# Kernel optimization log

Hardware: AMD Instinct MI355X
Metric: run time of the kernel (lower is better)

The kernel has to match this reference:

```python
import jax, jax.numpy as jnp
import numpy as np

N = 50000; FIN = 64; H = 128; E = 800000; T = 8
P = 250000; D = 500000; G = 20000; V = 2000; O = 2


def _mp(h, Ws, Wn, b, edge_src, edge_dst, n):
    # mean-aggregation message passing: relu(h Ws + mean_neigh(h) Wn + b)
    deg = jax.ops.segment_sum(jnp.ones(edge_dst.shape[0], h.dtype), edge_dst, n)
    agg = jax.ops.segment_sum(h[edge_src], edge_dst, n) / jnp.maximum(deg, 1.0)[:, None]
    return jax.nn.relu(h @ Ws + agg @ Wn + b)


def _forward(x, W_enc_self, W_enc_nei, b_enc, W2_self, W2_nei, b2, Wd1, bd1, Wd2, bd2,
             counts, edge_src, edge_dst, place_idx, src_idx, t_idx, dst_nodes, dst_seg,
             group_id, variant_of_group):
    n = x.shape[0]
    p = place_idx.shape[0]
    g = variant_of_group.shape[0]
    v = counts.shape[0]
    # first encoder, then T sequential second_encoder applications (feature generations)
    h0 = _mp(x, W_enc_self, W_enc_nei, b_enc, edge_src, edge_dst, n)

    def step(h, _):
        h2 = _mp(h, W2_self, W2_nei, b2, edge_src, edge_dst, n)
        return h2, h2

    _, hs = jax.lax.scan(step, h0, None, length=T)
    feats = jnp.concatenate([h0[None], hs], axis=0)  # [T+1, N, H]

    # gather (place, src) features at the generation index of each prediction
    place_f = feats[t_idx, place_idx]                 # [P, H]
    src_f = feats[t_idx, src_idx]                     # [P, H]
    # dst feature = sum over the destination set of each prediction
    dst_f = jax.ops.segment_sum(feats[t_idx[dst_seg], dst_nodes], dst_seg, p)  # [P, H]

    cat = jnp.concatenate([place_f, src_f, dst_f], axis=-1)  # [P, 3H]
    logits = jax.nn.relu(cat @ Wd1 + bd1) @ Wd2 + bd2        # [P, O]
    logprob = jax.nn.log_softmax(logits, axis=-1)            # [P, O]

    # prev_prob: inclusive running sum of per-step logprob sums within each variant
    group_sums = jax.ops.segment_sum(logprob, group_id, g)   # [G, O]
    cum = jnp.cumsum(group_sums, axis=0)
    var_tot = jax.ops.segment_sum(group_sums, variant_of_group, v)
    var_excl = jnp.cumsum(var_tot, axis=0) - var_tot
    within = cum - var_excl[variant_of_group]                # [G, O]
    prev = within[group_id]                                  # [P, O]

    logc = jnp.log(counts / jnp.sum(counts))                 # log(count/total) per variant
    add = logprob + prev + logc[variant_of_group[group_id]][:, None]
    return jnp.zeros((n, logits.shape[-1]), x.dtype).at[place_idx].add(add)


def setup_inputs() -> dict:
    ks = jax.random.split(jax.random.key(0), 24)
    s = jnp.float32(0.05)
    f32 = jnp.float32
    i32 = jnp.int32
    return {
        "x": jax.random.normal(ks[0], (N, FIN), f32),
        "W_enc_self": jax.random.normal(ks[1], (FIN, H), f32) * s,
        "W_enc_nei": jax.random.normal(ks[2], (FIN, H), f32) * s,
        "b_enc": jax.random.normal(ks[3], (H,), f32) * s,
        "W2_self": jax.random.normal(ks[4], (H, H), f32) * s,
        "W2_nei": jax.random.normal(ks[5], (H, H), f32) * s,
        "b2": jax.random.normal(ks[6], (H,), f32) * s,
        "Wd1": jax.random.normal(ks[7], (3 * H, 3 * H), f32) * s,
        "bd1": jax.random.normal(ks[8], (3 * H,), f32) * s,
        "Wd2": jax.random.normal(ks[9], (3 * H, O), f32) * s,
        "bd2": jax.random.normal(ks[10], (O,), f32) * s,
        "counts": jax.random.uniform(ks[11], (V,), f32) + 0.5,
        "edge_src": jax.random.randint(ks[12], (E,), 0, N, i32),
        "edge_dst": jax.random.randint(ks[13], (E,), 0, N, i32),
        "place_idx": jax.random.randint(ks[14], (P,), 0, N, i32),
        "src_idx": jax.random.randint(ks[15], (P,), 0, N, i32),
        "t_idx": jax.random.randint(ks[16], (P,), 0, T + 1, i32),
        "dst_nodes": jax.random.randint(ks[17], (D,), 0, N, i32),
        "dst_seg": jnp.sort(jax.random.randint(ks[18], (D,), 0, P, i32)),
        "group_id": jnp.sort(jax.random.randint(ks[19], (P,), 0, G, i32)),
        "variant_of_group": jnp.sort(jax.random.randint(ks[20], (G,), 0, V, i32)),
    }


def reference(x, W_enc_self, W_enc_nei, b_enc, W2_self, W2_nei, b2, Wd1, bd1, Wd2, bd2,
              counts, edge_src, edge_dst, place_idx, src_idx, t_idx, dst_nodes, dst_seg,
              group_id, variant_of_group):
    return _forward(x, W_enc_self, W_enc_nei, b_enc, W2_self, W2_nei, b2, Wd1, bd1, Wd2, bd2,
                    counts, edge_src, edge_dst, place_idx, src_idx, t_idx, dst_nodes, dst_seg,
                    group_id, variant_of_group)
```

## Files before the change

### kernel.cpp

```cpp
#include <hip/hip_runtime.h>
#include <math.h>

#define NN 50000
#define FINN 64
#define HD 128
#define EE 800000
#define TT 8
#define PP 250000
#define DD 500000
#define GG 20000
#define VV 2000
#define OO 2

#define DEC_GRID 256
#define DEC_TILES ((PP + 63) / 64)

typedef short short8 __attribute__((ext_vector_type(8)));
typedef float f32x4 __attribute__((ext_vector_type(4)));

__device__ __forceinline__ unsigned short f2bf(float f) {
    unsigned int u = __float_as_uint(f);
    u += 0x7fffu + ((u >> 16) & 1u);
    return (unsigned short)(u >> 16);
}
__device__ __forceinline__ float bf2f(unsigned short u) {
    return __uint_as_float(((unsigned int)u) << 16);
}

struct us8 { unsigned short v[8]; };

__device__ __forceinline__ void gload_lds16(const void* g, void* l) {
    __builtin_amdgcn_global_load_lds((__attribute__((address_space(1))) void*)g,
                                     (__attribute__((address_space(3))) void*)l, 16, 0, 0);
}

__global__ void count_k(const int* __restrict__ idx, int* __restrict__ counts, int n) {
    int i = blockIdx.x * blockDim.x + threadIdx.x;
    if (i < n) atomicAdd(&counts[idx[i]], 1);
}

__global__ void blk_sum_k(const int* __restrict__ counts, int n, int* __restrict__ bsum) {
    __shared__ int buf[256];
    int t = threadIdx.x, i = blockIdx.x * 256 + t;
    buf[t] = (i < n) ? counts[i] : 0;
    __syncthreads();
    for (int off = 128; off > 0; off >>= 1) {
        if (t < off) buf[t] += buf[t + off];
        __syncthreads();
    }
    if (t == 0) bsum[blockIdx.x] = buf[0];
}

__global__ void scan_small_k(const int* __restrict__ bsum, int nb, int* __restrict__ boff) {
    __shared__ int buf[256];
    int t = threadIdx.x;
    int v = (t < nb) ? bsum[t] : 0;
    buf[t] = v;
    __syncthreads();
    for (int off = 1; off < 256; off <<= 1) {
        int u = (t >= off) ? buf[t - off] : 0;
        __syncthreads();
        buf[t] += u;
        __syncthreads();
    }
    if (t < nb) boff[t] = buf[t] - v;
}

__global__ void rowptr_fill_k(const int* __restrict__ counts, const int* __restrict__ boff,
                              int n, int* __restrict__ rowptr, int total) {
    __shared__ int buf[256];
    int t = threadIdx.x, i = blockIdx.x * 256 + t;
    int v = (i < n) ? counts[i] : 0;
    buf[t] = v;
    __syncthreads();
    for (int off = 1; off < 256; off <<= 1) {
        int u = (t >= off) ? buf[t - off] : 0;
        __syncthreads();
        buf[t] += u;
        __syncthreads();
    }
    if (i < n) rowptr[i] = boff[blockIdx.x] + buf[t] - v;
    if (i == 0) rowptr[n] = total;
}

__global__ void lb_rowptr_k(const int* __restrict__ arr, int n, int* __restrict__ rowptr, int m) {
    int i = blockIdx.x * blockDim.x + threadIdx.x;
    if (i > m) return;
    int lo = 0, hi = n;
    while (lo < hi) {
        int mid = (lo + hi) >> 1;
        if (arr[mid] < i) lo = mid + 1; else hi = mid;
    }
    rowptr[i] = lo;
}

__global__ void fill_csr_k(const int* __restrict__ esrc, const int* __restrict__ edst,
                           const int* __restrict__ rowptr, int* __restrict__ cursor,
                           int* __restrict__ outi, int n) {
    int e = blockIdx.x * blockDim.x + threadIdx.x;
    if (e < n) {
        int d = edst[e];
        int pos = atomicAdd(&cursor[d], 1);
        outi[rowptr[d] + pos] = esrc[e];
    }
}

__global__ void hist9_k(const int* __restrict__ t_idx, int* __restrict__ hist) {
    __shared__ int l[9];
    if (threadIdx.x < 9) l[threadIdx.x] = 0;
    __syncthreads();
    int p = blockIdx.x * 256 + threadIdx.x;
    if (p < PP) atomicAdd(&l[t_idx[p]], 1);
    __syncthreads();
    if (threadIdx.x < 9) atomicAdd(&hist[threadIdx.x], l[threadIdx.x]);
}

__global__ void scan9_k(const int* __restrict__ hist, int* __restrict__ boff9) {
    if (threadIdx.x == 0) {
        int a = 0;
        for (int i = 0; i < 9; ++i) { boff9[i] = a; a += hist[i]; }
    }
}

__global__ void bucket_perm_k(const int* __restrict__ t_idx, const int* __restrict__ boff9,
                              int* __restrict__ cursor9, int* __restrict__ pperm) {
    __shared__ int lcnt[9];
    __shared__ int lbase[9];
    int tid = threadIdx.x;
    int p = blockIdx.x * 256 + tid;
    if (tid < 9) lcnt[tid] = 0;
    __syncthreads();
    int t = 0, lr = 0;
    bool ok = p < PP;
    if (ok) {
        t = t_idx[p];
        lr = atomicAdd(&lcnt[t], 1);
    }
    __syncthreads();
    if (tid < 9) lbase[tid] = atomicAdd(&cursor9[tid], lcnt[tid]);
    __syncthreads();
    if (ok) pperm[boff9[t] + lbase[t] + lr] = p;
}

__global__ void prep_k(const float* __restrict__ x,
                       const float* __restrict__ Wes, const float* __restrict__ Wen,
                       const float* __restrict__ W2s, const float* __restrict__ W2n,
                       const float* __restrict__ Wd1,
                       unsigned short* __restrict__ xb, unsigned short* __restrict__ wenc_t,
                       unsigned short* __restrict__ w2_t, unsigned short* __restrict__ wd1t) {
    int i = blockIdx.x * 256 + threadIdx.x;
    if (i < NN * FINN) xb[i] = f2bf(x[i]);
    if (i < HD * 2 * FINN) {
        int c = i / (2 * FINN), k = i - c * (2 * FINN);
        wenc_t[i] = f2bf((k < FINN) ? Wes[k * HD + c] : Wen[(k - FINN) * HD + c]);
    }
    if (i < HD * 2 * HD) {
        int c = i / (2 * HD), k = i - c * (2 * HD);
        w2_t[i] = f2bf((k < HD) ? W2s[k * HD + c] : W2n[(k - HD) * HD + c]);
    }
    if (i < 384 * 384) {
        int n = i / 384, k = i - n * 384;
        wd1t[i] = f2bf(Wd1[k * 384 + n]);
    }
}

template <int KIN>
__launch_bounds__(256)
__global__ void agg2_k(const unsigned short* __restrict__ h, const int* __restrict__ rowptr,
                       const int* __restrict__ csr_src, unsigned short* __restrict__ aggout) {
    constexpr int LPR = KIN >> 3;
    constexpr int EPW = 64 / LPR;
    int node = blockIdx.x * 4 + (threadIdx.x >> 6);
    int lane = threadIdx.x & 63;
    int sub = lane / LPR;
    int fl = lane % LPR;
    if (node >= NN) return;
    int s = rowptr[node], e = rowptr[node + 1];
    float acc[8] = {};
    int i = s + sub;
    int iB = i + EPW;
    int srcA = (i < e) ? csr_src[i] : 0;
    int srcB = (iB < e) ? csr_src[iB] : 0;
    while (i < e) {
        bool hB = iB < e;
        us8 vA = *(const us8*)&h[(size_t)srcA * KIN + fl * 8];
        us8 vB;
        if (hB) vB = *(const us8*)&h[(size_t)srcB * KIN + fl * 8];
        int iN = iB + EPW, iN2 = iN + EPW;
        srcA = (iN < e) ? csr_src[iN] : 0;
        srcB = (iN2 < e) ? csr_src[iN2] : 0;
#pragma unroll
        for (int j = 0; j < 8; ++j) acc[j] += bf2f(vA.v[j]);
        if (hB) {
#pragma unroll
            for (int j = 0; j < 8; ++j) acc[j] += bf2f(vB.v[j]);
        }
        i = iN; iB = iN2;
    }
#pragma unroll
    for (int m = LPR; m < 64; m <<= 1)
#pragma unroll
        for (int j = 0; j < 8; ++j) acc[j] += __shfl_xor(acc[j], m);
    if (sub == 0) {
        float d = fmaxf((float)(e - s), 1.f);
        us8 o;
#pragma unroll
        for (int j = 0; j < 8; ++j) o.v[j] = f2bf(acc[j] / d);
        *(us8*)&aggout[(size_t)node * KIN + fl * 8] = o;
    }
}

__launch_bounds__(128)
__global__ void mp_mfma_k(const unsigned short* __restrict__ hin,
                          const unsigned short* __restrict__ aggin,
                          const unsigned short* __restrict__ Wt,
                          const float* __restrict__ bias,
                          unsigned short* __restrict__ hout, int Kin) {
    int tid = threadIdx.x;
    int lane = tid & 63, w = tid >> 6;
    int cc = lane & 15, g = lane >> 4;
    int K = 2 * Kin;
    int rowA = blockIdx.x * 32 + w * 16 + cc;
    bool rowok = rowA < NN;
    const unsigned short* hrow = hin + (size_t)rowA * Kin;
    const unsigned short* arow = aggin + (size_t)rowA * Kin;

    f32x4 acc[8];
#pragma unroll
    for (int t = 0; t < 8; ++t) acc[t] = (f32x4){0.f, 0.f, 0.f, 0.f};

    for (int k0 = 0; k0 < K; k0 += 32) {
        int k = k0 + g * 8;
        short8 a = {0, 0, 0, 0, 0, 0, 0, 0};
        if (rowok)
            a = *(const short8*)((k < Kin) ? (hrow + k) : (arow + (k - Kin)));
#pragma unroll
        for (int t = 0; t < 8; ++t) {
            short8 b = *(const short8*)&Wt[(size_t)(t * 16 + cc) * K + k];
            acc[t] = __builtin_amdgcn_mfma_f32_16x16x32_bf16(a, b, acc[t], 0, 0, 0);
        }
    }
#pragma unroll
    for (int t = 0; t < 8; ++t) {
        int col = t * 16 + cc;
        float b1 = bias[col];
#pragma unroll
        for (int r = 0; r < 4; ++r) {
            int grow = blockIdx.x * 32 + w * 16 + g * 4 + r;
            if (grow < NN)
                hout[(size_t)grow * HD + col] = f2bf(fmaxf(acc[t][r] + b1, 0.f));
        }
    }
}

__launch_bounds__(256)
__global__ void dst_sum_k(const unsigned short* __restrict__ feats,
                          const int* __restrict__ t_idx, const int* __restrict__ dst_nodes,
                          const int* __restrict__ dst_rowptr, const int* __restrict__ pperm,
                          unsigned short* __restrict__ dstc) {
    int pi = blockIdx.x * 4 + (threadIdx.x >> 6);
    int lane = threadIdx.x & 63;
    int sub = lane >> 4;
    int fl = lane & 15;
    if (pi >= PP) return;
    int p = pperm[pi];
    long t = t_idx[p];
    const unsigned short* base = feats + t * (long)NN * HD;
    int s = dst_rowptr[p], e = dst_rowptr[p + 1];
    float acc[8] = {};
    int i = s + sub;
    int nd_next = (i < e) ? dst_nodes[i] : 0;
    for (; i < e; i += 4) {
        int nd = nd_next;
        int in = i + 4;
        if (in < e) nd_next = dst_nodes[in];
        us8 v = *(const us8*)&base[(size_t)nd * HD + fl * 8];
#pragma unroll
        for (int j = 0; j < 8; ++j) acc[j] += bf2f(v.v[j]);
    }
#pragma unroll
    for (int m = 16; m < 64; m <<= 1)
#pragma unroll
        for (int j = 0; j < 8; ++j) acc[j] += __shfl_xor(acc[j], m);
    if (sub == 0) {
        us8 o;
#pragma unroll
        for (int j = 0; j < 8; ++j) o.v[j] = f2bf(acc[j]);
        *(us8*)&dstc[(size_t)pi * HD + fl * 8] = o;
    }
}

__launch_bounds__(256, 1)
__global__ void dec4_k(const unsigned short* __restrict__ feats,
                       const unsigned short* __restrict__ dstc,
                       const int* __restrict__ place_idx, const int* __restrict__ src_idx,
                       const int* __restrict__ t_idx, const int* __restrict__ group_id,
                       const int* __restrict__ pperm,
                       const unsigned short* __restrict__ Wd1t,
                       const float* __restrict__ bd1, const float* __restrict__ Wd2,
                       const float* __restrict__ bd2, float* __restrict__ logprob,
                       float* __restrict__ group_sums) {
    __shared__ unsigned short buf[2][192 * 128];
    __shared__ unsigned long long rb[2][192];
    __shared__ float lpart[4][64][2];

    int tid = threadIdx.x;
    int lane = tid & 63, w = tid >> 6;
    int cc = lane & 15, gq = lane >> 4;
    int cx7 = cc & 7;
    int bid = blockIdx.x;

    int row = min(tid, 191);
    int sec = row >> 6, pl = row & 63;
    const int* nptr = (sec == 0) ? place_idx : src_idx;

    int nt = (DEC_TILES - 1 - bid) / DEC_GRID + 1;

    int pic0 = min(bid * 64 + pl, PP - 1);
    int pic1 = min((bid + DEC_GRID) * 64 + pl, PP - 1);
    int pic2p = min((bid + 2 * DEC_GRID) * 64 + pl, PP - 1);
    int pA = pperm[pic0], pB = pperm[pic1];
    int preg = pperm[pic2p];
    int tA = t_idx[pA], tB = t_idx[pB];
    int nA = nptr[pA], nB = nptr[pB];
    if (tid < 192) {
        rb[0][tid] = (sec == 2) ? (unsigned long long)(dstc + (size_t)pic0 * HD)
                                : (unsigned long long)(feats + (((long)tA * NN + nA) * (long)HD));
        rb[1][tid] = (sec == 2) ? (unsigned long long)(dstc + (size_t)pic1 * HD)
                                : (unsigned long long)(feats + (((long)tB * NN + nB) * (long)HD));
    }

    short8 breg[72];
    {
        const unsigned short* bbase = Wd1t + ((long)(w * 96 + cc) * 384 + gq * 8);
#pragma unroll
        for (int kk = 0; kk < 12; ++kk)
#pragma unroll
            for (int t = 0; t < 6; ++t)
                breg[kk * 6 + t] = *(const short8*)(bbase + (long)t * 16 * 384 + kk * 32);
    }
    __syncthreads();

    int rsub = lane >> 4, chunk = lane & 15;

#define STAGE(par_)                                                                  \
    {                                                                                \
        _Pragma("unroll")                                                            \
        for (int i = 0; i < 12; ++i) {                                               \
            int r = w * 48 + i * 4 + rsub;                                           \
            const unsigned short* src =                                              \
                (const unsigned short*)rb[par_][r] + ((chunk ^ (r & 7)) * 8);        \
            gload_lds16(src, &buf[par_][(w * 48 + i * 4) * 128]);                    \
        }                                                                            \
    }

    STAGE(0);

    for (int k = 0; k < nt; ++k) {
        int par = k & 1, npar = par ^ 1;
        int tl = bid + k * DEC_GRID;

        int tload = t_idx[preg];
        int nload = nptr[preg];
        int pic3v = min((bid + (k + 3) * DEC_GRID) * 64 + pl, PP - 1);
        int preg2 = pperm[pic3v];
        int pic2v = min((bid + (k + 2) * DEC_GRID) * 64 + pl, PP - 1);

        STAGE(npar);

        __builtin_amdgcn_sched_barrier(0);
        asm volatile("s_waitcnt vmcnt(15)" ::: "memory");
        __builtin_amdgcn_s_barrier();
        __builtin_amdgcn_sched_barrier(0);

        const unsigned short* bufc = &buf[par][0];
        f32x4 acc[4][6];
#pragma unroll
        for (int s = 0; s < 4; ++s)
#pragma unroll
            for (int t = 0; t < 6; ++t) acc[s][t] = (f32x4){0.f, 0.f, 0.f, 0.f};

#pragma unroll
        for (int kk = 0; kk < 12; ++kk) {
            int seck = kk >> 2;
            int cbase = (kk & 3) * 4 + gq;
            int coff = (cbase ^ cx7) * 8;
            short8 a_c[4];
#pragma unroll
            for (int s = 0; s < 4; ++s) {
                int lrow = seck * 64 + s * 16 + cc;
                a_c[s] = *(const short8*)&bufc[lrow * 128 + coff];
            }
#pragma unroll
            for (int t = 0; t < 6; ++t)
#pragma unroll
                for (int s = 0; s < 4; ++s)
                    acc[s][t] = __builtin_amdgcn_mfma_f32_16x16x32_bf16(a_c[s], breg[kk * 6 + t],
                                                                        acc[s][t], 0, 0, 0);
        }

        float part[4][4][2] = {};
#pragma unroll
        for (int t = 0; t < 6; ++t) {
            int col = w * 96 + t * 16 + cc;
            float b1 = bd1[col];
            float w0 = Wd2[col * 2 + 0], w1 = Wd2[col * 2 + 1];
#pragma unroll
            for (int s = 0; s < 4; ++s)
#pragma unroll
                for (int r = 0; r < 4; ++r) {
                    float h = fmaxf(acc[s][t][r] + b1, 0.f);
                    part[s][r][0] += h * w0;
                    part[s][r][1] += h * w1;
                }
        }
#pragma unroll
        for (int m = 1; m < 16; m <<= 1)
#pragma unroll
            for (int s = 0; s < 4; ++s)
#pragma unroll
                for (int r = 0; r < 4; ++r) {
                    part[s][r][0] += __shfl_xor(part[s][r][0], m);
                    part[s][r][1] += __shfl_xor(part[s][r][1], m);
                }
        if (cc == 0) {
#pragma unroll
            for (int s = 0; s < 4; ++s)
#pragma unroll
                for (int r = 0; r < 4; ++r) {
                    int orow = s * 16 + gq * 4 + r;
                    lpart[w][orow][0] = part[s][r][0];
                    lpart[w][orow][1] = part[s][r][1];
                }
        }

        if (tid < 192)
            rb[par][tid] = (sec == 2)
                               ? (unsigned long long)(dstc + (size_t)pic2v * HD)
                               : (unsigned long long)(feats + (((long)tload * NN + nload) * (long)HD));
        preg = preg2;

        asm volatile("s_waitcnt lgkmcnt(0)" ::: "memory");
        __builtin_amdgcn_s_barrier();
        __builtin_amdgcn_sched_barrier(0);

        if (tid < 64) {
            int pi = tl * 64 + tid;
            if (pi < PP) {
                int p = pperm[pi];
                float l0 = lpart[0][tid][0] + lpart[1][tid][0] + lpart[2][tid][0] +
                           lpart[3][tid][0] + bd2[0];
                float l1 = lpart[0][tid][1] + lpart[1][tid][1] + lpart[2][tid][1] +
                           lpart[3][tid][1] + bd2[1];
                float m = fmaxf(l0, l1);
                float lse = m + logf(expf(l0 - m) + expf(l1 - m));
                float lp0 = l0 - lse, lp1 = l1 - lse;
                logprob[p * 2 + 0] = lp0;
                logprob[p * 2 + 1] = lp1;
                int g = group_id[p];
                atomicAdd(&group_sums[g * 2 + 0], lp0);
                atomicAdd(&group_sums[g * 2 + 1], lp1);
            }
        }
    }
#undef STAGE
}

__global__ void within_total_k(const float* __restrict__ group_sums,
                               const int* __restrict__ var_rowptr,
                               const float* __restrict__ counts,
                               float* __restrict__ within, float* __restrict__ total) {
    __shared__ float buf[256];
    int tid = threadIdx.x;
    float s = 0.f;
    for (int i = tid; i < VV; i += 256) s += counts[i];
    buf[tid] = s;
    __syncthreads();
    for (int off = 128; off > 0; off >>= 1) {
        if (tid < off) buf[tid] += buf[tid + off];
        __syncthreads();
    }
    if (tid == 0) total[0] = buf[0];
    for (int v = tid; v < VV; v += 256) {
        int gs = var_rowptr[v], ge = var_rowptr[v + 1];
        float r0 = 0.f, r1 = 0.f;
        for (int g = gs; g < ge; ++g) {
            r0 += group_sums[2 * g + 0];
            r1 += group_sums[2 * g + 1];
            within[2 * g + 0] = r0;
            within[2 * g + 1] = r1;
        }
    }
}

__global__ void final_k(const float* __restrict__ logprob, const float* __restrict__ within,
                        const int* __restrict__ group_id, const int* __restrict__ vog,
                        const float* __restrict__ counts, const float* __restrict__ total,
                        const int* __restrict__ place_idx, float* __restrict__ outp) {
    int p = blockIdx.x * blockDim.x + threadIdx.x;
    if (p >= PP) return;
    int g = group_id[p];
    int v = vog[g];
    float lc = logf(counts[v]) - logf(total[0]);
    int node = place_idx[p];
    atomicAdd(&outp[node * 2 + 0], logprob[p * 2 + 0] + within[g * 2 + 0] + lc);
    atomicAdd(&outp[node * 2 + 1], logprob[p * 2 + 1] + within[g * 2 + 1] + lc);
}

extern "C" void kernel_launch(void* const* d_in, const int* in_sizes, int n_in,
                              void* d_out, int out_size, void* d_ws, size_t ws_size,
                              hipStream_t stream) {
    const float* x          = (const float*)d_in[0];
    const float* W_enc_self = (const float*)d_in[1];
    const float* W_enc_nei  = (const float*)d_in[2];
    const float* b_enc      = (const float*)d_in[3];
    const float* W2_self    = (const float*)d_in[4];
    const float* W2_nei     = (const float*)d_in[5];
    const float* b2         = (const float*)d_in[6];
    const float* Wd1        = (const float*)d_in[7];
    const float* bd1        = (const float*)d_in[8];
    const float* Wd2        = (const float*)d_in[9];
    const float* bd2        = (const float*)d_in[10];
    const float* counts     = (const float*)d_in[11];
    const int* edge_src     = (const int*)d_in[12];
    const int* edge_dst     = (const int*)d_in[13];
    const int* place_idx    = (const int*)d_in[14];
    const int* src_idx      = (const int*)d_in[15];
    const int* t_idx        = (const int*)d_in[16];
    const int* dst_nodes    = (const int*)d_in[17];
    const int* dst_seg      = (const int*)d_in[18];
    const int* group_id     = (const int*)d_in[19];
    const int* variant_of_group = (const int*)d_in[20];
    float* outp = (float*)d_out;

    const int NB = (NN + 255) / 256;

    unsigned short* feats = (unsigned short*)d_ws;
    unsigned short* aggb  = feats + (size_t)(TT + 1) * NN * HD;
    unsigned short* xb    = aggb + (size_t)NN * HD;
    unsigned short* dstc  = xb + (size_t)NN * FINN;
    unsigned short* wenc_t = dstc + (size_t)PP * HD;
    unsigned short* w2_t   = wenc_t + HD * 2 * FINN;
    unsigned short* wd1t   = w2_t + HD * 2 * HD;
    int* zr = (int*)(wd1t + 384 * 384);
    int* csr_counts   = zr;
    int* csr_cursor   = csr_counts + NN;
    float* group_sums = (float*)(csr_cursor + NN);
    int* hist9        = (int*)(group_sums + 2 * GG);
    int* cursor9      = hist9 + 9;
    size_t zero_words = (size_t)NN + NN + 2 * GG + 18;
    int* bsum       = cursor9 + 9;
    int* boff       = bsum + 256;
    int* boff9      = boff + 256;
    int* csr_rowptr = boff9 + 16;
    int* dst_rowptr = csr_rowptr + (NN + 1);
    int* var_rowptr = dst_rowptr + (PP + 1);
    int* csr_src    = var_rowptr + (VV + 1);
    int* pperm      = csr_src + EE;
    float* logprob  = (float*)(pperm + PP);
    float* within   = logprob + 2 * PP;
    float* total_counts = within + 2 * GG;

    hipMemsetAsync(zr, 0, zero_words * 4, stream);
    hipMemsetAsync(d_out, 0, (size_t)out_size * sizeof(float), stream);

    prep_k<<<(NN * FINN + 255) / 256, 256, 0, stream>>>(x, W_enc_self, W_enc_nei, W2_self,
                                                        W2_nei, Wd1, xb, wenc_t, w2_t, wd1t);
    count_k<<<(EE + 255) / 256, 256, 0, stream>>>(edge_dst, csr_counts, EE);
    blk_sum_k<<<NB, 256, 0, stream>>>(csr_counts, NN, bsum);
    scan_small_k<<<1, 256, 0, stream>>>(bsum, NB, boff);
    rowptr_fill_k<<<NB, 256, 0, stream>>>(csr_counts, boff, NN, csr_rowptr, EE);
    fill_csr_k<<<(EE + 255) / 256, 256, 0, stream>>>(edge_src, edge_dst, csr_rowptr,
                                                     csr_cursor, csr_src, EE);
    lb_rowptr_k<<<(PP + 256) / 256, 256, 0, stream>>>(dst_seg, DD, dst_rowptr, PP);
    lb_rowptr_k<<<(VV + 256) / 256, 256, 0, stream>>>(variant_of_group, GG, var_rowptr, VV);
    hist9_k<<<(PP + 255) / 256, 256, 0, stream>>>(t_idx, hist9);
    scan9_k<<<1, 64, 0, stream>>>(hist9, boff9);
    bucket_perm_k<<<(PP + 255) / 256, 256, 0, stream>>>(t_idx, boff9, cursor9, pperm);

    for (int r = 0; r <= TT; ++r) {
        const unsigned short* hin = (r == 0) ? xb : feats + (size_t)(r - 1) * NN * HD;
        unsigned short* hout = feats + (size_t)r * NN * HD;
        if (r == 0) {
            agg2_k<FINN><<<(NN + 3) / 4, 256, 0, stream>>>(hin, csr_rowptr, csr_src, aggb);
            mp_mfma_k<<<(NN + 31) / 32, 128, 0, stream>>>(hin, aggb, wenc_t, b_enc, hout, FINN);
        } else {
            agg2_k<HD><<<(NN + 3) / 4, 256, 0, stream>>>(hin, csr_rowptr, csr_src, aggb);
            mp_mfma_k<<<(NN + 31) / 32, 128, 0, stream>>>(hin, aggb, w2_t, b2, hout, HD);
        }
    }

    dst_sum_k<<<(PP + 3) / 4, 256, 0, stream>>>(feats, t_idx, dst_nodes, dst_rowptr, pperm, dstc);
    dec4_k<<<DEC_GRID, 256, 0, stream>>>(feats, dstc, place_idx, src_idx, t_idx,
                                         group_id, pperm, wd1t, bd1, Wd2, bd2,
                                         logprob, group_sums);

    within_total_k<<<1, 256, 0, stream>>>(group_sums, var_rowptr, counts, within, total_counts);
    final_k<<<(PP + 255) / 256, 256, 0, stream>>>(logprob, within, group_id, variant_of_group,
                                                  counts, total_counts, place_idx, outp);
}
```

Measured before the change: 1.084 ms.

## Triple-buffer decoder staging, defer softmax epilogue, use 16 lanes per dst row

The decoder kernel moves from double to triple buffering of the gathered LDS tiles, prefetching two tiles ahead with adjusted vmcnt waits. The log-softmax and atomic epilogue is deferred one iteration, using a double-buffered partial-logit array and spread across all four waves, so it overlaps with the next tile's MFMA work. The dst-sum kernel now gives each prediction one 16-lane group that walks its whole segment two rows at a time, replacing the four-way split and cross-lane shuffle reduction. The added LDS buffer raises shared memory use to about 150KB per block, and the tuned vmcnt counts are fragile.

```diff
diff --git a/kernel.cpp b/kernel.cpp
--- a/kernel.cpp
+++ b/kernel.cpp
@@ -254,44 +254,47 @@
 }
 
 __launch_bounds__(256)
-__global__ void dst_sum_k(const unsigned short* __restrict__ feats,
-                          const int* __restrict__ t_idx, const int* __restrict__ dst_nodes,
-                          const int* __restrict__ dst_rowptr, const int* __restrict__ pperm,
-                          unsigned short* __restrict__ dstc) {
-    int pi = blockIdx.x * 4 + (threadIdx.x >> 6);
-    int lane = threadIdx.x & 63;
-    int sub = lane >> 4;
-    int fl = lane & 15;
+__global__ void dst_sum2_k(const unsigned short* __restrict__ feats,
+                           const int* __restrict__ t_idx, const int* __restrict__ dst_nodes,
+                           const int* __restrict__ dst_rowptr, const int* __restrict__ pperm,
+                           unsigned short* __restrict__ dstc) {
+    int tid = threadIdx.x;
+    int grp = tid >> 4;
+    int fl = tid & 15;
+    int pi = blockIdx.x * 16 + grp;
     if (pi >= PP) return;
     int p = pperm[pi];
     long t = t_idx[p];
     const unsigned short* base = feats + t * (long)NN * HD;
     int s = dst_rowptr[p], e = dst_rowptr[p + 1];
     float acc[8] = {};
-    int i = s + sub;
-    int nd_next = (i < e) ? dst_nodes[i] : 0;
-    for (; i < e; i += 4) {
-        int nd = nd_next;
-        int in = i + 4;
-        if (in < e) nd_next = dst_nodes[in];
-        us8 v = *(const us8*)&base[(size_t)nd * HD + fl * 8];
-#pragma unroll
-        for (int j = 0; j < 8; ++j) acc[j] += bf2f(v.v[j]);
-    }
-#pragma unroll
-    for (int m = 16; m < 64; m <<= 1)
-#pragma unroll
-        for (int j = 0; j < 8; ++j) acc[j] += __shfl_xor(acc[j], m);
-    if (sub == 0) {
-        us8 o;
-#pragma unroll
-        for (int j = 0; j < 8; ++j) o.v[j] = f2bf(acc[j]);
-        *(us8*)&dstc[(size_t)pi * HD + fl * 8] = o;
-    }
+    int i = s;
+    int n0 = (i < e) ? dst_nodes[i] : 0;
+    int n1 = (i + 1 < e) ? dst_nodes[i + 1] : 0;
+    while (i < e) {
+        bool h1 = (i + 1) < e;
+        us8 v0 = *(const us8*)&base[(size_t)n0 * HD + fl * 8];
+        us8 v1;
+        if (h1) v1 = *(const us8*)&base[(size_t)n1 * HD + fl * 8];
+        int i2 = i + 2, i3 = i + 3;
+        n0 = (i2 < e) ? dst_nodes[i2] : 0;
+        n1 = (i3 < e) ? dst_nodes[i3] : 0;
+#pragma unroll
+        for (int j = 0; j < 8; ++j) acc[j] += bf2f(v0.v[j]);
+        if (h1) {
+#pragma unroll
+            for (int j = 0; j < 8; ++j) acc[j] += bf2f(v1.v[j]);
+        }
+        i = i2;
+    }
+    us8 o;
+#pragma unroll
+    for (int j = 0; j < 8; ++j) o.v[j] = f2bf(acc[j]);
+    *(us8*)&dstc[(size_t)pi * HD + fl * 8] = o;
 }
 
 __launch_bounds__(256, 1)
-__global__ void dec4_k(const unsigned short* __restrict__ feats,
+__global__ void dec5_k(const unsigned short* __restrict__ feats,
                        const unsigned short* __restrict__ dstc,
                        const int* __restrict__ place_idx, const int* __restrict__ src_idx,
                        const int* __restrict__ t_idx, const int* __restrict__ group_id,
@@ -300,9 +303,9 @@
                        const float* __restrict__ bd1, const float* __restrict__ Wd2,
                        const float* __restrict__ bd2, float* __restrict__ logprob,
                        float* __restrict__ group_sums) {
-    __shared__ unsigned short buf[2][192 * 128];
-    __shared__ unsigned long long rb[2][192];
-    __shared__ float lpart[4][64][2];
+    __shared__ unsigned short buf[3][192 * 128];
+    __shared__ unsigned long long rb[3][192];
+    __shared__ float lpart[2][4][64][2];
 
     int tid = threadIdx.x;
     int lane = tid & 63, w = tid >> 6;
@@ -316,18 +319,20 @@
 
     int nt = (DEC_TILES - 1 - bid) / DEC_GRID + 1;
 
-    int pic0 = min(bid * 64 + pl, PP - 1);
-    int pic1 = min((bid + DEC_GRID) * 64 + pl, PP - 1);
-    int pic2p = min((bid + 2 * DEC_GRID) * 64 + pl, PP - 1);
-    int pA = pperm[pic0], pB = pperm[pic1];
-    int preg = pperm[pic2p];
-    int tA = t_idx[pA], tB = t_idx[pB];
-    int nA = nptr[pA], nB = nptr[pB];
+    float b20 = bd2[0], b21 = bd2[1];
+
+    int pic0 = min((bid + 0 * DEC_GRID) * 64 + pl, PP - 1);
+    int pic1 = min((bid + 1 * DEC_GRID) * 64 + pl, PP - 1);
+    int pic2 = min((bid + 2 * DEC_GRID) * 64 + pl, PP - 1);
+    int pA = pperm[pic0], pB = pperm[pic1], pC = pperm[pic2];
+    int preg = pperm[min((bid + 3 * DEC_GRID) * 64 + pl, PP - 1)];
     if (tid < 192) {
         rb[0][tid] = (sec == 2) ? (unsigned long long)(dstc + (size_t)pic0 * HD)
-                                : (unsigned long long)(feats + (((long)tA * NN + nA) * (long)HD));
+                                : (unsigned long long)(feats + (((long)t_idx[pA] * NN + nptr[pA]) * (long)HD));
         rb[1][tid] = (sec == 2) ? (unsigned long long)(dstc + (size_t)pic1 * HD)
-                                : (unsigned long long)(feats + (((long)tB * NN + nB) * (long)HD));
+                                : (unsigned long long)(feats + (((long)t_idx[pB] * NN + nptr[pB]) * (long)HD));
+        rb[2][tid] = (sec == 2) ? (unsigned long long)(dstc + (size_t)pic2 * HD)
+                                : (unsigned long long)(feats + (((long)t_idx[pC] * NN + nptr[pC]) * (long)HD));
     }
 
     short8 breg[72];
@@ -343,35 +348,66 @@
 
     int rsub = lane >> 4, chunk = lane & 15;
 
-#define STAGE(par_)                                                                  \
+#define STAGE(slot_)                                                                 \
     {                                                                                \
         _Pragma("unroll")                                                            \
         for (int i = 0; i < 12; ++i) {                                               \
             int r = w * 48 + i * 4 + rsub;                                           \
             const unsigned short* src =                                              \
-                (const unsigned short*)rb[par_][r] + ((chunk ^ (r & 7)) * 8);        \
-            gload_lds16(src, &buf[par_][(w * 48 + i * 4) * 128]);                    \
+                (const unsigned short*)rb[slot_][r] + ((chunk ^ (r & 7)) * 8);       \
+            gload_lds16(src, &buf[slot_][(w * 48 + i * 4) * 128]);                   \
         }                                                                            \
     }
 
+#define OUTPUT(tlo_, po_)                                                            \
+    if (lane < 16) {                                                                 \
+        int orow = w * 16 + cc;                                                      \
+        int pi = (tlo_) * 64 + orow;                                                 \
+        if (pi < PP) {                                                               \
+            int p = pperm[pi];                                                       \
+            float l0 = lpart[po_][0][orow][0] + lpart[po_][1][orow][0] +             \
+                       lpart[po_][2][orow][0] + lpart[po_][3][orow][0] + b20;        \
+            float l1 = lpart[po_][0][orow][1] + lpart[po_][1][orow][1] +             \
+                       lpart[po_][2][orow][1] + lpart[po_][3][orow][1] + b21;        \
+            float mm = fmaxf(l0, l1);                                                \
+            float lse = mm + logf(expf(l0 - mm) + expf(l1 - mm));                    \
+            float lp0 = l0 - lse, lp1 = l1 - lse;                                    \
+            logprob[p * 2 + 0] = lp0;                                                \
+            logprob[p * 2 + 1] = lp1;                                                \
+            int g = group_id[p];                                                     \
+            atomicAdd(&group_sums[g * 2 + 0], lp0);                                  \
+            atomicAdd(&group_sums[g * 2 + 1], lp1);                                  \
+        }                                                                            \
+    }
+
     STAGE(0);
+    STAGE(1);
 
     for (int k = 0; k < nt; ++k) {
-        int par = k & 1, npar = par ^ 1;
-        int tl = bid + k * DEC_GRID;
+        int par = k % 3;
 
         int tload = t_idx[preg];
         int nload = nptr[preg];
-        int pic3v = min((bid + (k + 3) * DEC_GRID) * 64 + pl, PP - 1);
-        int preg2 = pperm[pic3v];
-        int pic2v = min((bid + (k + 2) * DEC_GRID) * 64 + pl, PP - 1);
-
-        STAGE(npar);
+        int preg2 = pperm[min((bid + (k + 4) * DEC_GRID) * 64 + pl, PP - 1)];
+        int picw = min((bid + (k + 3) * DEC_GRID) * 64 + pl, PP - 1);
+
+        if (k + 2 < nt) STAGE((k + 2) % 3);
 
         __builtin_amdgcn_sched_barrier(0);
-        asm volatile("s_waitcnt vmcnt(15)" ::: "memory");
+        if (k + 2 < nt) {
+            asm volatile("s_waitcnt vmcnt(27)" ::: "memory");
+        } else if (k + 1 < nt) {
+            asm volatile("s_waitcnt vmcnt(18)" ::: "memory");
+        } else {
+            asm volatile("s_waitcnt vmcnt(6)" ::: "memory");
+        }
         __builtin_amdgcn_s_barrier();
         __builtin_amdgcn_sched_barrier(0);
+
+        if (k > 0) {
+            int tprev = bid + (k - 1) * DEC_GRID;
+            OUTPUT(tprev, (k - 1) & 1);
+        }
 
         const unsigned short* bufc = &buf[par][0];
         f32x4 acc[4][6];
@@ -429,41 +465,28 @@
 #pragma unroll
                 for (int r = 0; r < 4; ++r) {
                     int orow = s * 16 + gq * 4 + r;
-                    lpart[w][orow][0] = part[s][r][0];
-                    lpart[w][orow][1] = part[s][r][1];
+                    lpart[k & 1][w][orow][0] = part[s][r][0];
+                    lpart[k & 1][w][orow][1] = part[s][r][1];
                 }
         }
 
         if (tid < 192)
             rb[par][tid] = (sec == 2)
-                               ? (unsigned long long)(dstc + (size_t)pic2v * HD)
+                               ? (unsigned long long)(dstc + (size_t)picw * HD)
                                : (unsigned long long)(feats + (((long)tload * NN + nload) * (long)HD));
         preg = preg2;
 
         asm volatile("s_waitcnt lgkmcnt(0)" ::: "memory");
         __builtin_amdgcn_s_barrier();
         __builtin_amdgcn_sched_barrier(0);
-
-        if (tid < 64) {
-            int pi = tl * 64 + tid;
-            if (pi < PP) {
-                int p = pperm[pi];
-                float l0 = lpart[0][tid][0] + lpart[1][tid][0] + lpart[2][tid][0] +
-                           lpart[3][tid][0] + bd2[0];
-                float l1 = lpart[0][tid][1] + lpart[1][tid][1] + lpart[2][tid][1] +
-                           lpart[3][tid][1] + bd2[1];
-                float m = fmaxf(l0, l1);
-                float lse = m + logf(expf(l0 - m) + expf(l1 - m));
-                float lp0 = l0 - lse, lp1 = l1 - lse;
-                logprob[p * 2 + 0] = lp0;
-                logprob[p * 2 + 1] = lp1;
-                int g = group_id[p];
-                atomicAdd(&group_sums[g * 2 + 0], lp0);
-                atomicAdd(&group_sums[g * 2 + 1], lp1);
-            }
-        }
+    }
+
+    {
+        int tlast = bid + (nt - 1) * DEC_GRID;
+        OUTPUT(tlast, (nt - 1) & 1);
     }
 #undef STAGE
+#undef OUTPUT
 }
 
 __global__ void within_total_k(const float* __restrict__ group_sums,
@@ -590,8 +613,8 @@
         }
     }
 
-    dst_sum_k<<<(PP + 3) / 4, 256, 0, stream>>>(feats, t_idx, dst_nodes, dst_rowptr, pperm, dstc);
-    dec4_k<<<DEC_GRID, 256, 0, stream>>>(feats, dstc, place_idx, src_idx, t_idx,
+    dst_sum2_k<<<(PP + 15) / 16, 256, 0, stream>>>(feats, t_idx, dst_nodes, dst_rowptr, pperm, dstc);
+    dec5_k<<<DEC_GRID, 256, 0, stream>>>(feats, dstc, place_idx, src_idx, t_idx,
                                          group_id, pperm, wd1t, bd1, Wd2, bd2,
                                          logprob, group_sums);
 
```

Result: faster. 1.049 ms (-3.3%).
